# Kernel optimization log

Measured on AMD Instinct MI355X. Metric: run time of the kernel, lower is better.

Reference implementation:

```python
import jax, jax.numpy as jnp
import numpy as np

N_EMBEDDING = 32
HEAD_SIZE = 64
B, T = 8, 4096


def setup_inputs() -> dict:
    key = jax.random.key(0)
    kx, kk, kq, kv = jax.random.split(key, 4)
    x = jax.random.normal(kx, (B, T, N_EMBEDDING), dtype=jnp.float32)
    Wk = jax.random.normal(kk, (N_EMBEDDING, HEAD_SIZE), dtype=jnp.float32) * 0.05
    Wq = jax.random.normal(kq, (N_EMBEDDING, HEAD_SIZE), dtype=jnp.float32) * 0.05
    Wv = jax.random.normal(kv, (N_EMBEDDING, HEAD_SIZE), dtype=jnp.float32) * 0.05
    return {"x": x, "Wk": Wk, "Wq": Wq, "Wv": Wv}


def reference(x, Wk, Wq, Wv):
    # x: [B, T, C]; projections (no bias)
    k = jnp.einsum("btc,cd->btd", x, Wk)  # [B,T,D]
    q = jnp.einsum("btc,cd->btd", x, Wq)
    v = jnp.einsum("btc,cd->btd", x, Wv)
    # raw scores (NOTE: original module applies no 1/sqrt(D) scaling)
    wei = jnp.einsum("bqd,bkd->bqk", q, k)  # [B,T,T]
    t = x.shape[1]
    causal = jnp.tril(jnp.ones((t, t), dtype=bool))
    wei = jnp.where(causal[None, :, :], wei, -jnp.inf)
    wei = jax.nn.softmax(wei, axis=-1)
    out = jnp.einsum("bqk,bkd->bqd", wei, v)  # [B,T,D]
    return out
```

## Files before the change

kernel.cpp:

```cpp
#include <hip/hip_runtime.h>
#include <hip/hip_bf16.h>

constexpr int Bc = 8;
constexpr int Tt = 4096;
constexpr int Dd = 64;

typedef __attribute__((ext_vector_type(8))) short short8;
typedef __attribute__((ext_vector_type(4))) float floatx4;
typedef __attribute__((ext_vector_type(4))) __fp16 half4;
typedef __attribute__((ext_vector_type(2))) __fp16 half2v;
typedef uint4   __attribute__((may_alias)) uint4_a;
typedef short8  __attribute__((may_alias)) short8_a;
typedef ushort4 __attribute__((may_alias)) ushort4_a;
typedef float4  __attribute__((may_alias)) float4_a;
typedef half4   __attribute__((may_alias)) half4_a;

#define MFMA16(A, B, C)  __builtin_amdgcn_mfma_f32_16x16x32_bf16(A, B, C, 0, 0, 0)
#define MFMAH16(A, B, C) __builtin_amdgcn_mfma_f32_16x16x16f16(A, B, C, 0, 0, 0)
constexpr float LOG2E = 1.4426950408889634f;

constexpr size_t XB_OFF = 0;
constexpr size_t YB_OFF = (size_t)2 << 20;
constexpr size_t XT_OFF = (size_t)4 << 20;
constexpr size_t WV_OFF = (size_t)6 << 20;

__device__ __forceinline__ unsigned rnd16(float x) {
    unsigned u; __builtin_memcpy(&u, &x, 4); return u + 0x8000u;
}
__device__ __forceinline__ unsigned pk_bf2(float lo, float hi) {
    return __builtin_amdgcn_perm(rnd16(hi), rnd16(lo), 0x07060302);
}
__device__ __forceinline__ ushort4 pack4(floatx4 d) {
    union { unsigned u[2]; ushort4 v; } r;
    r.u[0] = pk_bf2(d[0], d[1]);
    r.u[1] = pk_bf2(d[2], d[3]);
    return r.v;
}
__device__ __forceinline__ short8 cvt8(float4 a, float4 b) {
    union { unsigned u[4]; short8 s; } r;
    r.u[0] = pk_bf2(a.x, a.y);
    r.u[1] = pk_bf2(a.z, a.w);
    r.u[2] = pk_bf2(b.x, b.y);
    r.u[3] = pk_bf2(b.z, b.w);
    return r.s;
}

__global__ __launch_bounds__(256) void prep_kernel(
    const float* __restrict__ x,
    const float* __restrict__ Wk, const float* __restrict__ Wq,
    const float* __restrict__ Wv,
    char* __restrict__ ws)
{
    __shared__ uint4 sG[128];
    __shared__ float sX[2048];

    const int bi = blockIdx.x;
    const int b = bi >> 6, ch = bi & 63;
    const int tid = threadIdx.x;
    const int wave = tid >> 6, lane = tid & 63;
    const int ln15 = lane & 15, quad = lane >> 4;
    const size_t bT = (size_t)b * Tt;
    const int r0 = ch * 64;

    const int lr = wave * 16 + ln15;
    const float* xp = x + (bT + r0 + lr) * 32 + quad * 8;
    float4 pX0 = ((const float4_a*)xp)[0];
    float4 pX1 = ((const float4_a*)xp)[1];
    *(float4_a*)(&sX[lr * 32 + quad * 8])     = pX0;
    *(float4_a*)(&sX[lr * 32 + quad * 8 + 4]) = pX1;

    if (wave == 0) {
        floatx4 gC[2][2];
        #pragma unroll
        for (int mt = 0; mt < 2; ++mt)
            #pragma unroll
            for (int nt = 0; nt < 2; ++nt) gC[mt][nt] = (floatx4){0.f,0.f,0.f,0.f};
        #pragma unroll
        for (int kt = 0; kt < 2; ++kt) {
            short8 aG[2], bG[2];
            #pragma unroll
            for (int mt = 0; mt < 2; ++mt) {
                const float* qp = Wq + (ln15 + 16*mt)*64 + 32*kt + quad*8;
                float4 a = ((const float4_a*)qp)[0], bb = ((const float4_a*)qp)[1];
                a.x*=LOG2E; a.y*=LOG2E; a.z*=LOG2E; a.w*=LOG2E;
                bb.x*=LOG2E; bb.y*=LOG2E; bb.z*=LOG2E; bb.w*=LOG2E;
                aG[mt] = cvt8(a, bb);
                const float* kp = Wk + (ln15 + 16*mt)*64 + 32*kt + quad*8;
                bG[mt] = cvt8(((const float4_a*)kp)[0], ((const float4_a*)kp)[1]);
            }
            #pragma unroll
            for (int mt = 0; mt < 2; ++mt)
                #pragma unroll
                for (int nt = 0; nt < 2; ++nt)
                    gC[mt][nt] = MFMA16(aG[mt], bG[nt], gC[mt][nt]);
        }
        unsigned short* sGh = (unsigned short*)sG;
        #pragma unroll
        for (int mt = 0; mt < 2; ++mt)
            #pragma unroll
            for (int nt = 0; nt < 2; ++nt)
                *(ushort4_a*)(sGh + (16*nt + ln15)*32 + 16*mt + quad*4)
                    = pack4(gC[mt][nt]);
    }
    __syncthreads();

    union { unsigned u[4]; uint4 v; } xu;
    xu.u[0] = pk_bf2(pX0.x, pX0.y); xu.u[1] = pk_bf2(pX0.z, pX0.w);
    xu.u[2] = pk_bf2(pX1.x, pX1.y); xu.u[3] = pk_bf2(pX1.z, pX1.w);
    *(uint4_a*)(ws + XB_OFF + (size_t)(bT + r0 + lr) * 64 + quad * 16) = xu.v;

    {
        short8 xq = cvt8(pX0, pX1);
        unsigned short* yb = (unsigned short*)(ws + YB_OFF);
        #pragma unroll
        for (int mt = 0; mt < 2; ++mt) {
            union { uint4 u; short8 s; } g;
            g.u = sG[(16*mt + ln15)*4 + quad];
            floatx4 d = (floatx4){0.f,0.f,0.f,0.f};
            d = MFMA16(g.s, xq, d);
            *(ushort4_a*)(yb + (size_t)(bT + r0 + lr) * 32 + 16*mt + quad*4)
                = pack4(d);
        }
    }

    {
        const int kc = tid >> 6;
        const int c = (tid >> 1) & 31, kh = tid & 1;
        float v[8];
        #pragma unroll
        for (int j = 0; j < 8; ++j) v[j] = sX[(kc*16 + kh*8 + j)*32 + c];
        union { unsigned u[4]; uint4 q; } x4;
        #pragma unroll
        for (int j = 0; j < 4; ++j) {
            union { half2v h; unsigned u; } p;
            p.h = __builtin_amdgcn_cvt_pkrtz(v[2*j], v[2*j+1]);
            x4.u[j] = p.u;
        }
        *(uint4_a*)(ws + XT_OFF
                    + ((size_t)((b*256 + ch*4 + kc) * 32 + c)) * 32 + kh * 16)
            = x4.q;
    }

    if (bi == 0 && wave == 2) {
        const int d = lane;
        unsigned short* wvb = (unsigned short*)(ws + WV_OFF);
        float v[32];
        #pragma unroll
        for (int c2 = 0; c2 < 32; ++c2) v[c2] = Wv[c2*64 + d];
        #pragma unroll
        for (int i2 = 0; i2 < 16; ++i2)
            ((unsigned*)(wvb + d*32))[i2] = pk_bf2(v[2*i2], v[2*i2+1]);
    }
}

__global__ __launch_bounds__(512, 2) void attn_kernel(
    const char* __restrict__ ws, float* __restrict__ out)
{
    __shared__ float4 sZm[2][4][4][2][64];
    __shared__ float  sLm[2][4][4][64];
    __shared__ uint4  sB4[8][64];

    const int b = blockIdx.x & 7;
    const int u = blockIdx.x >> 3;
    const int tid = threadIdx.x;
    const int wave = tid >> 6, lane = tid & 63;
    const int h = wave >> 2, kg = wave & 3;
    const int ln15 = lane & 15, quad = lane >> 4;
    const size_t bT = (size_t)b * Tt;

    const int qt = h ? u : (63 - u);
    const int q0 = qt * 64;

    const char* xbB = ws + XB_OFF + bT * 64;
    const char* xtB = ws + XT_OFF + (size_t)b * (256 * 1024);
    const int aOff = ln15 * 64 + quad * 16;
    const int xOff = ln15 * 32 + quad * 8;

    short8 bq[4];
    #pragma unroll
    for (int nt = 0; nt < 4; ++nt) {
        union { uint4 u4; short8 s; } t0;
        t0.u4 = *(const uint4_a*)(ws + YB_OFF
                 + (size_t)(bT + q0 + 16*nt + ln15) * 64 + quad * 16);
        bq[nt] = t0.s;
    }

    floatx4 z4[4][2];
    float lq[4];
    #pragma unroll
    for (int nt = 0; nt < 4; ++nt) {
        z4[nt][0] = (floatx4){0.f,0.f,0.f,0.f};
        z4[nt][1] = (floatx4){0.f,0.f,0.f,0.f};
        lq[nt] = 0.f;
    }

    short8 aA[4], aB4[4];

    auto LDA = [&](int k, short8* a) {
        const char* p = xbB + (size_t)k * 4096 + aOff;
        #pragma unroll
        for (int t = 0; t < 4; ++t)
            a[t] = *(const short8_a*)(p + t * 1024);
    };

    auto BODY = [&](int kt, const short8* a) {
        const char* px = xtB + (size_t)kt * 4096 + xOff;
        half4 xa[8];
        #pragma unroll
        for (int t = 0; t < 4; ++t) {
            xa[2*t]   = *(const half4_a*)(px + t * 1024);
            xa[2*t+1] = *(const half4_a*)(px + t * 1024 + 512);
        }
        __builtin_amdgcn_sched_barrier(0);
        #pragma unroll
        for (int nt = 0; nt < 4; ++nt) {
            floatx4 s4[4];
            #pragma unroll
            for (int t = 0; t < 4; ++t) {
                floatx4 c0 = (floatx4){0.f,0.f,0.f,0.f};
                s4[t] = MFMA16(a[t], bq[nt], c0);
            }
            if (kt == qt) {
                const int qrow = q0 + 16*nt + ln15;
                #pragma unroll
                for (int t = 0; t < 4; ++t) {
                    const int keyb = kt*64 + 16*t + quad*4;
                    #pragma unroll
                    for (int r = 0; r < 4; ++r) {
                        float p = (keyb + r <= qrow)
                                  ? __builtin_amdgcn_exp2f(s4[t][r]) : 0.f;
                        s4[t][r] = p; lq[nt] += p;
                    }
                }
            } else {
                #pragma unroll
                for (int t = 0; t < 4; ++t)
                    #pragma unroll
                    for (int r = 0; r < 4; ++r) {
                        float p = __builtin_amdgcn_exp2f(s4[t][r]);
                        s4[t][r] = p; lq[nt] += p;
                    }
            }
            #pragma unroll
            for (int t = 0; t < 4; ++t) {
                union { half2v h2[2]; half4 h4; } pb;
                pb.h2[0] = __builtin_amdgcn_cvt_pkrtz(s4[t][0], s4[t][1]);
                pb.h2[1] = __builtin_amdgcn_cvt_pkrtz(s4[t][2], s4[t][3]);
                z4[nt][0] = MFMAH16(xa[2*t],   pb.h4, z4[nt][0]);
                z4[nt][1] = MFMAH16(xa[2*t+1], pb.h4, z4[nt][1]);
            }
        }
    };

    int kt = kg;
    if (kt <= qt) {
        LDA(kt, aA);
        while (true) {
            int kn = kt + 4;
            LDA(kn <= qt ? kn : kt, aB4);
            BODY(kt, aA);
            if (kn > qt) break;
            kt = kn; kn = kt + 4;
            LDA(kn <= qt ? kn : kt, aA);
            BODY(kt, aB4);
            if (kn > qt) break;
            kt = kn;
        }
    }

    #pragma unroll
    for (int nt = 0; nt < 4; ++nt) {
        sZm[h][nt][kg][0][lane] = make_float4(z4[nt][0][0], z4[nt][0][1],
                                              z4[nt][0][2], z4[nt][0][3]);
        sZm[h][nt][kg][1][lane] = make_float4(z4[nt][1][0], z4[nt][1][1],
                                              z4[nt][1][2], z4[nt][1][3]);
        sLm[h][nt][kg][lane] = lq[nt];
    }
    __syncthreads();

    {
        const int nt = kg;
        float4 zm0 = make_float4(0.f,0.f,0.f,0.f);
        float4 zm1 = make_float4(0.f,0.f,0.f,0.f);
        float l = 0.f;
        #pragma unroll
        for (int g = 0; g < 4; ++g) {
            float4 a0 = sZm[h][nt][g][0][lane];
            float4 a1 = sZm[h][nt][g][1][lane];
            zm0.x+=a0.x; zm0.y+=a0.y; zm0.z+=a0.z; zm0.w+=a0.w;
            zm1.x+=a1.x; zm1.y+=a1.y; zm1.z+=a1.z; zm1.w+=a1.w;
            l += sLm[h][nt][g][lane];
        }
        l += __shfl_xor(l, 16);
        l += __shfl_xor(l, 32);
        const float inv = 1.f / l;

        const unsigned short* wvb = (const unsigned short*)(ws + WV_OFF);
        short8 wv_f[4];
        #pragma unroll
        for (int t = 0; t < 4; ++t) {
            union { uint4 u4; short8 s; } w0;
            w0.u4 = *(const uint4_a*)(wvb + (16*t + ln15) * 32 + quad * 8);
            wv_f[t] = w0.s;
        }
        unsigned short* sZb = (unsigned short*)&sB4[wave][0];
        floatx4 zv0 = (floatx4){zm0.x, zm0.y, zm0.z, zm0.w};
        floatx4 zv1 = (floatx4){zm1.x, zm1.y, zm1.z, zm1.w};
        *(ushort4_a*)(sZb + ln15*32 + quad*4)      = pack4(zv0);
        *(ushort4_a*)(sZb + ln15*32 + 16 + quad*4) = pack4(zv1);
        union { uint4 u4; short8 s; } zb;
        zb.u4 = sB4[wave][ln15*4 + quad];
        const int qrow = q0 + 16*nt + ln15;
        #pragma unroll
        for (int t = 0; t < 4; ++t) {
            floatx4 o = (floatx4){0.f,0.f,0.f,0.f};
            o = MFMA16(wv_f[t], zb.s, o);
            *(float4_a*)(out + (bT + (size_t)qrow) * Dd + 16*t + quad*4)
                = make_float4(o[0]*inv, o[1]*inv, o[2]*inv, o[3]*inv);
        }
    }
}

extern "C" void kernel_launch(void* const* d_in, const int* in_sizes, int n_in,
                              void* d_out, int out_size, void* d_ws, size_t ws_size,
                              hipStream_t stream)
{
    const float* x  = (const float*)d_in[0];
    const float* Wk = (const float*)d_in[1];
    const float* Wq = (const float*)d_in[2];
    const float* Wv = (const float*)d_in[3];
    float* out = (float*)d_out;

    prep_kernel<<<512, 256, 0, stream>>>(x, Wk, Wq, Wv, (char*)d_ws);
    attn_kernel<<<Bc * 32, 512, 0, stream>>>((const char*)d_ws, out);
}
```

Before: 85.58 us.

## Use one query tile per block with eight key-split waves

Each block previously paired a short and a long causal query tile, two halves of four waves each. Now each block handles a single query tile and splits its key tiles across all eight waves, launching twice as many blocks. The launch bound is raised to request four blocks per multiprocessor, and the epilogue is split so each wave reduces one row tile and computes half of the output columns. This trades the explicit pairing-based load balance for finer-grained key splitting and higher occupancy, which risks register pressure and uneven block lengths across the grid.

New measurement: 116.0 us. +35.6%, slower.

```diff
diff --git a/kernel.cpp b/kernel.cpp
--- a/kernel.cpp
+++ b/kernel.cpp
@@ -153,22 +153,20 @@
     }
 }
 
-__global__ __launch_bounds__(512, 2) void attn_kernel(
+__global__ __launch_bounds__(512, 4) void attn_kernel(
     const char* __restrict__ ws, float* __restrict__ out)
 {
-    __shared__ float4 sZm[2][4][4][2][64];
-    __shared__ float  sLm[2][4][4][64];
+    __shared__ float4 sZm[4][8][2][64];
+    __shared__ float  sLm[4][8][64];
     __shared__ uint4  sB4[8][64];
 
-    const int b = blockIdx.x & 7;
-    const int u = blockIdx.x >> 3;
+    const int b  = blockIdx.x & 7;
+    const int qt = blockIdx.x >> 3;
     const int tid = threadIdx.x;
     const int wave = tid >> 6, lane = tid & 63;
-    const int h = wave >> 2, kg = wave & 3;
+    const int kg = wave;
     const int ln15 = lane & 15, quad = lane >> 4;
     const size_t bT = (size_t)b * Tt;
-
-    const int qt = h ? u : (63 - u);
     const int q0 = qt * 64;
 
     const char* xbB = ws + XB_OFF + bT * 64;
@@ -256,11 +254,11 @@
     if (kt <= qt) {
         LDA(kt, aA);
         while (true) {
-            int kn = kt + 4;
+            int kn = kt + 8;
             LDA(kn <= qt ? kn : kt, aB4);
             BODY(kt, aA);
             if (kn > qt) break;
-            kt = kn; kn = kt + 4;
+            kt = kn; kn = kt + 8;
             LDA(kn <= qt ? kn : kt, aA);
             BODY(kt, aB4);
             if (kn > qt) break;
@@ -270,38 +268,39 @@
 
     #pragma unroll
     for (int nt = 0; nt < 4; ++nt) {
-        sZm[h][nt][kg][0][lane] = make_float4(z4[nt][0][0], z4[nt][0][1],
-                                              z4[nt][0][2], z4[nt][0][3]);
-        sZm[h][nt][kg][1][lane] = make_float4(z4[nt][1][0], z4[nt][1][1],
-                                              z4[nt][1][2], z4[nt][1][3]);
-        sLm[h][nt][kg][lane] = lq[nt];
+        sZm[nt][kg][0][lane] = make_float4(z4[nt][0][0], z4[nt][0][1],
+                                           z4[nt][0][2], z4[nt][0][3]);
+        sZm[nt][kg][1][lane] = make_float4(z4[nt][1][0], z4[nt][1][1],
+                                           z4[nt][1][2], z4[nt][1][3]);
+        sLm[nt][kg][lane] = lq[nt];
     }
     __syncthreads();
 
     {
-        const int nt = kg;
+        const int nt = kg & 3, th = kg >> 2;
         float4 zm0 = make_float4(0.f,0.f,0.f,0.f);
         float4 zm1 = make_float4(0.f,0.f,0.f,0.f);
         float l = 0.f;
         #pragma unroll
-        for (int g = 0; g < 4; ++g) {
-            float4 a0 = sZm[h][nt][g][0][lane];
-            float4 a1 = sZm[h][nt][g][1][lane];
+        for (int g = 0; g < 8; ++g) {
+            float4 a0 = sZm[nt][g][0][lane];
+            float4 a1 = sZm[nt][g][1][lane];
             zm0.x+=a0.x; zm0.y+=a0.y; zm0.z+=a0.z; zm0.w+=a0.w;
             zm1.x+=a1.x; zm1.y+=a1.y; zm1.z+=a1.z; zm1.w+=a1.w;
-            l += sLm[h][nt][g][lane];
+            l += sLm[nt][g][lane];
         }
         l += __shfl_xor(l, 16);
         l += __shfl_xor(l, 32);
         const float inv = 1.f / l;
 
         const unsigned short* wvb = (const unsigned short*)(ws + WV_OFF);
-        short8 wv_f[4];
-        #pragma unroll
-        for (int t = 0; t < 4; ++t) {
+        short8 wv_f[2];
+        #pragma unroll
+        for (int tt = 0; tt < 2; ++tt) {
+            const int t = 2*th + tt;
             union { uint4 u4; short8 s; } w0;
             w0.u4 = *(const uint4_a*)(wvb + (16*t + ln15) * 32 + quad * 8);
-            wv_f[t] = w0.s;
+            wv_f[tt] = w0.s;
         }
         unsigned short* sZb = (unsigned short*)&sB4[wave][0];
         floatx4 zv0 = (floatx4){zm0.x, zm0.y, zm0.z, zm0.w};
@@ -312,9 +311,10 @@
         zb.u4 = sB4[wave][ln15*4 + quad];
         const int qrow = q0 + 16*nt + ln15;
         #pragma unroll
-        for (int t = 0; t < 4; ++t) {
+        for (int tt = 0; tt < 2; ++tt) {
+            const int t = 2*th + tt;
             floatx4 o = (floatx4){0.f,0.f,0.f,0.f};
-            o = MFMA16(wv_f[t], zb.s, o);
+            o = MFMA16(wv_f[tt], zb.s, o);
             *(float4_a*)(out + (bT + (size_t)qrow) * Dd + 16*t + quad*4)
                 = make_float4(o[0]*inv, o[1]*inv, o[2]*inv, o[3]*inv);
         }
@@ -332,5 +332,5 @@
     float* out = (float*)d_out;
 
     prep_kernel<<<512, 256, 0, stream>>>(x, Wk, Wq, Wv, (char*)d_ws);
-    attn_kernel<<<Bc * 32, 512, 0, stream>>>((const char*)d_ws, out);
-}
+    attn_kernel<<<Bc * 64, 512, 0, stream>>>((const char*)d_ws, out);
+}
```
